# Kernel optimization log

Measured on AMD Instinct MI355X. Metric: run time of the kernel, lower is better.

Reference implementation:

```python
import jax, jax.numpy as jnp
import numpy as np

N_NODES = 50000
N_EDGES = 800000
N_GRAPHS = 512


def gcn_conv(x, W, b, src, dst, n_nodes):
    # Standard PyG GCNConv: linear transform, add self-loops, D^-1/2 (A+I) D^-1/2 aggregation.
    x = x @ W  # [N, out]
    loop = jnp.arange(n_nodes, dtype=src.dtype)
    s = jnp.concatenate([src, loop])  # [E+N]
    d = jnp.concatenate([dst, loop])
    deg = jax.ops.segment_sum(jnp.ones_like(d, dtype=x.dtype), d, num_segments=n_nodes)
    dinv = jnp.where(deg > 0, jax.lax.rsqrt(jnp.maximum(deg, 1e-12)), 0.0)
    norm = dinv[s] * dinv[d]  # [E+N]
    msg = x[s] * norm[:, None]  # gather + scale
    out = jax.ops.segment_sum(msg, d, num_segments=n_nodes)  # scatter-add
    return out + b


def setup_inputs() -> dict:
    key = jax.random.key(0)
    ks = jax.random.split(key, 10)
    x = jax.random.normal(ks[0], (N_NODES, 128), dtype=jnp.float32)
    edge_index = jax.random.randint(ks[1], (2, N_EDGES), 0, N_NODES, dtype=jnp.int64)
    batch = jnp.sort(jax.random.randint(ks[2], (N_NODES,), 0, N_GRAPHS, dtype=jnp.int64))
    y = jax.random.randint(ks[3], (N_GRAPHS,), 0, 4, dtype=jnp.int64)
    W1 = jax.random.normal(ks[4], (128, 64), dtype=jnp.float32) * (1.0 / np.sqrt(128))
    b1 = jnp.zeros((64,), dtype=jnp.float32)
    W2 = jax.random.normal(ks[5], (64, 64), dtype=jnp.float32) * (1.0 / np.sqrt(64))
    b2 = jnp.zeros((64,), dtype=jnp.float32)
    Wfc = jax.random.normal(ks[6], (64, 4), dtype=jnp.float32) * (1.0 / np.sqrt(64))
    bfc = jnp.zeros((4,), dtype=jnp.float32)
    return {"x": x, "edge_index": edge_index, "batch": batch, "y": y,
            "W1": W1, "b1": b1, "W2": W2, "b2": b2, "Wfc": Wfc, "bfc": bfc}


def reference(x, edge_index, batch, y, W1, b1, W2, b2, Wfc, bfc):
    src, dst = edge_index[0], edge_index[1]
    h = jax.nn.relu(gcn_conv(x, W1, b1, src, dst, N_NODES))
    h = jax.nn.relu(gcn_conv(h, W2, b2, src, dst, N_NODES))
    # global mean pool over graph ids
    sums = jax.ops.segment_sum(h, batch, num_segments=N_GRAPHS)  # [G, out]
    cnts = jax.ops.segment_sum(jnp.ones((h.shape[0],), h.dtype), batch, num_segments=N_GRAPHS)
    pooled = sums / jnp.maximum(cnts, 1.0)[:, None]
    logits = pooled @ Wfc + bfc
    logp = jax.nn.log_softmax(logits, axis=1)
    return (logp, y)
```

## Files before the change

### kernel.cpp

```cpp
#include <hip/hip_runtime.h>
#include <hip/hip_fp16.h>
#include <math.h>

#define N_NODES 50000
#define N_EDGES 800000
#define N_GRAPHS 512
#define NBKT 196
#define SENT N_NODES
#define CAP_T 6144
#define CAP_S 8192

typedef float v2f __attribute__((ext_vector_type(2)));

#define OFF_BCNT    0u
#define OFF_DINV    1024u
#define OFF_OFFS2   201216u
#define OFF_TMP     601344u
#define OFF_SORTED  5418240u
#define OFF_XS8_1   11840768u
#define OFF_XS8_2   15041024u
#define OFF_H2      18241280u

__global__ __launch_bounds__(256) void binA(const int* __restrict__ src, const int* __restrict__ dst,
                                            int* __restrict__ bcnt, unsigned int* __restrict__ tmp,
                                            unsigned int* __restrict__ x1, unsigned int* __restrict__ x2) {
    __shared__ int cnt[256];
    __shared__ int lo[256];
    __shared__ int cnt2[256];
    __shared__ int baseg[256];
    __shared__ unsigned int ldsPK[4096];
    __shared__ int ldsDST[4096];
    int t = threadIdx.x;
    cnt[t] = 0; cnt2[t] = 0;
    if (blockIdx.x == 0) {
        if (t < 16) x1[N_NODES * 16 + t] = 0;
        else if (t < 32) x2[N_NODES * 16 + (t - 16)] = 0;
    }
    __syncthreads();
    int e0 = blockIdx.x * 4096;
    int nE = N_EDGES - e0; if (nE > 4096) nE = 4096;
    int sA[16], dA[16];
#pragma unroll
    for (int i = 0; i < 16; ++i) {
        int e = e0 + i * 256 + t;
        if (e < N_EDGES) {
            sA[i] = src[e];
            dA[i] = dst[e];
            atomicAdd(&cnt[dA[i] >> 8], 1);
        } else dA[i] = -1;
    }
    __syncthreads();
    {
        int v = cnt[t];
        lo[t] = v;
        __syncthreads();
        for (int d = 1; d < 256; d <<= 1) {
            int a = (t >= d) ? lo[t - d] : 0;
            __syncthreads();
            lo[t] += a;
            __syncthreads();
        }
        int ex = lo[t] - v;
        __syncthreads();
        lo[t] = ex;
        baseg[t] = (t < NBKT && v) ? atomicAdd(&bcnt[t], v) : 0;
    }
    __syncthreads();
#pragma unroll
    for (int i = 0; i < 16; ++i) {
        if (dA[i] >= 0) {
            int b = dA[i] >> 8;
            int pl = lo[b] + atomicAdd(&cnt2[b], 1);
            ldsPK[pl] = (unsigned int)sA[i] | ((unsigned int)(dA[i] & 255) << 17);
            ldsDST[pl] = b * CAP_T + baseg[b] + (pl - lo[b]);
        }
    }
    __syncthreads();
    for (int p = t; p < nE; p += 256)
        tmp[ldsDST[p]] = ldsPK[p];
}

__global__ __launch_bounds__(256) void binB2(const unsigned int* __restrict__ tmp,
                                             const int* __restrict__ bcnt,
                                             int* __restrict__ sorted, int2* __restrict__ offs2,
                                             float* __restrict__ dinv) {
    __shared__ int cnt[256];
    __shared__ int scn[256];
    __shared__ int cur[256];
    __shared__ int ldsS[CAP_S];
    int b = blockIdx.x, t = threadIdx.x;
    cnt[t] = 0;
    __syncthreads();
    int m = bcnt[b];
    const unsigned int* tp = tmp + b * CAP_T;
    for (int e = t; e < m; e += 256) atomicAdd(&cnt[tp[e] >> 17], 1);
    __syncthreads();
    int deg = cnt[t];
    int pdeg = (deg + 7) & ~7;
    scn[t] = pdeg;
    __syncthreads();
    for (int d = 1; d < 256; d <<= 1) {
        int a = (t >= d) ? scn[t - d] : 0;
        __syncthreads();
        scn[t] += a;
        __syncthreads();
    }
    int begl = scn[t] - pdeg;
    int ptot = scn[255];
    int node = b * 256 + t;
    if (node < N_NODES) {
        offs2[node] = make_int2(b * CAP_S + begl, b * CAP_S + begl + pdeg);
        dinv[node] = rsqrtf(1.0f + (float)deg);
    }
    cur[t] = begl;
    __syncthreads();
    for (int e = t; e < m; e += 256) {
        unsigned int pk = tp[e];
        int p = atomicAdd(&cur[pk >> 17], 1);
        ldsS[p] = (int)(pk & 0x1FFFFu);
    }
    __syncthreads();
    for (int p = cur[t]; p < begl + pdeg; ++p) ldsS[p] = SENT;
    __syncthreads();
    int4* dst4 = (int4*)(sorted + b * CAP_S);
    const int4* src4 = (const int4*)ldsS;
    for (int p = t; p < (ptot >> 2); p += 256) dst4[p] = src4[p];
}

__global__ __launch_bounds__(256) void gemm1(const float* __restrict__ X, const float* __restrict__ W,
                                             const float* __restrict__ dinv, unsigned int* __restrict__ xs8) {
    __shared__ float sW[128 * 64];
    __shared__ float sX[16 * 132];
    int tid = threadIdx.x;
    {
        const float4* ws = (const float4*)W;
        float4* wd = (float4*)sW;
        for (int i = tid; i < 2048; i += 256) wd[i] = ws[i];
    }
    int row0 = blockIdx.x * 16;
    {
        const float4* xs = (const float4*)(X + row0 * 128);
        for (int i = tid; i < 512; i += 256) {
            int r = i >> 5, q = i & 31;
            *(float4*)&sX[r * 132 + 4 * q] = xs[r * 32 + q];
        }
    }
    __syncthreads();
    int r = tid >> 4;
    int cg = (tid & 15) * 4;
    int row = row0 + r;
    float a0 = 0, a1 = 0, a2 = 0, a3 = 0;
#pragma unroll 8
    for (int k = 0; k < 128; ++k) {
        float xv = sX[r * 132 + k];
        float4 w = *(const float4*)&sW[k * 64 + cg];
        a0 += xv * w.x; a1 += xv * w.y; a2 += xv * w.z; a3 += xv * w.w;
    }
    float s = dinv[row];
    unsigned int pk = 0;
    pk = __builtin_amdgcn_cvt_pk_fp8_f32(a0 * s, a1 * s, pk, false);
    pk = __builtin_amdgcn_cvt_pk_fp8_f32(a2 * s, a3 * s, pk, true);
    xs8[row * 16 + (cg >> 2)] = pk;
}

#define ADD_ROW(rv) { \
    v2f f0 = __builtin_amdgcn_cvt_pk_f32_fp8((rv).x, false); \
    v2f f1 = __builtin_amdgcn_cvt_pk_f32_fp8((rv).x, true); \
    v2f f2 = __builtin_amdgcn_cvt_pk_f32_fp8((rv).y, false); \
    v2f f3 = __builtin_amdgcn_cvt_pk_f32_fp8((rv).y, true); \
    a0 += f0.x; a1 += f0.y; a2 += f1.x; a3 += f1.y; \
    a4 += f2.x; a5 += f2.y; a6 += f3.x; a7 += f3.y; }

#define RED_SUB() { \
    a0 += __shfl_xor(a0, 8);  a1 += __shfl_xor(a1, 8);  a2 += __shfl_xor(a2, 8);  a3 += __shfl_xor(a3, 8); \
    a4 += __shfl_xor(a4, 8);  a5 += __shfl_xor(a5, 8);  a6 += __shfl_xor(a6, 8);  a7 += __shfl_xor(a7, 8); \
    a0 += __shfl_xor(a0, 16); a1 += __shfl_xor(a1, 16); a2 += __shfl_xor(a2, 16); a3 += __shfl_xor(a3, 16); \
    a4 += __shfl_xor(a4, 16); a5 += __shfl_xor(a5, 16); a6 += __shfl_xor(a6, 16); a7 += __shfl_xor(a7, 16); \
    a0 += __shfl_xor(a0, 32); a1 += __shfl_xor(a1, 32); a2 += __shfl_xor(a2, 32); a3 += __shfl_xor(a3, 32); \
    a4 += __shfl_xor(a4, 32); a5 += __shfl_xor(a5, 32); a6 += __shfl_xor(a6, 32); a7 += __shfl_xor(a7, 32); }

#define GATHER_BODY(FLUSH_ADV) \
    int lane = threadIdx.x & 63; \
    int sub = lane >> 3, frag = lane & 7; \
    int n0 = wv * 4; \
    int2 oe = offs2[n0 + (lane < 4 ? lane : 3)]; \
    int e0 = __shfl(oe.x, 0), e1 = __shfl(oe.x, 1), e2 = __shfl(oe.x, 2); \
    int e3 = __shfl(oe.x, 3), e4 = __shfl(oe.y, 3); \
    int G   = (e4 - e0) >> 3; \
    int nb1 = (e1 - e0) >> 3, nb2 = (e2 - e0) >> 3, nb3 = (e3 - e0) >> 3; \
    const int* sb = sorted + e0 + sub; \
    int i0 = (0 < G) ? sb[0]  : SENT; \
    int i1 = (1 < G) ? sb[8]  : SENT; \
    int i2 = (2 < G) ? sb[16] : SENT; \
    int i3 = (3 < G) ? sb[24] : SENT; \
    float4 bA = *(const float4*)(bias + frag * 8); \
    float4 bB = *(const float4*)(bias + frag * 8 + 4); \
    int cur = 0; \
    uint2 sv = *(const uint2*)(xs8 + n0 * 64 + frag * 8); \
    float dv = dinv[n0]; \
    float a0 = 0, a1 = 0, a2 = 0, a3 = 0, a4 = 0, a5 = 0, a6 = 0, a7 = 0; \
    for (int g = 0; g < G; g += 4) { \
        uint2 r0 = *(const uint2*)(xs8 + i0 * 64 + frag * 8); \
        uint2 r1 = *(const uint2*)(xs8 + i1 * 64 + frag * 8); \
        uint2 r2 = *(const uint2*)(xs8 + i2 * 64 + frag * 8); \
        uint2 r3 = *(const uint2*)(xs8 + i3 * 64 + frag * 8); \
        const int* np = sb + (g + 4) * 8; \
        i0 = (g + 4 < G) ? np[0]  : SENT; \
        i1 = (g + 5 < G) ? np[8]  : SENT; \
        i2 = (g + 6 < G) ? np[16] : SENT; \
        i3 = (g + 7 < G) ? np[24] : SENT; \
        {   int gg = g; \
            int nxt = BND_NXT(); \
            while (cur < 4 && gg >= nxt) { FLUSH_ADV(); nxt = BND_NXT(); } \
            ADD_ROW(r0); } \
        if (g + 1 < G) { \
            int gg = g + 1; \
            int nxt = BND_NXT(); \
            while (cur < 4 && gg >= nxt) { FLUSH_ADV(); nxt = BND_NXT(); } \
            ADD_ROW(r1); \
        } \
        if (g + 2 < G) { \
            int gg = g + 2; \
            int nxt = BND_NXT(); \
            while (cur < 4 && gg >= nxt) { FLUSH_ADV(); nxt = BND_NXT(); } \
            ADD_ROW(r2); \
        } \
        if (g + 3 < G) { \
            int gg = g + 3; \
            int nxt = BND_NXT(); \
            while (cur < 4 && gg >= nxt) { FLUSH_ADV(); nxt = BND_NXT(); } \
            ADD_ROW(r3); \
        } \
    } \
    while (cur < 4) { FLUSH_ADV(); }

#define BND_NXT() (cur == 0 ? nb1 : cur == 1 ? nb2 : cur == 2 ? nb3 : G)

__global__ __launch_bounds__(256) void gather_fuse(const unsigned char* __restrict__ xs8,
                                                   const int2* __restrict__ offs2,
                                                   const int* __restrict__ sorted,
                                                   const float* __restrict__ dinv,
                                                   const float* __restrict__ bias,
                                                   const float* __restrict__ W2,
                                                   unsigned int* __restrict__ xs8o) {
    __shared__ float sW2[64 * 64];
    __shared__ float sH[16][64];
    {
        const float4* ws = (const float4*)W2;
        float4* wd = (float4*)sW2;
        for (int i = threadIdx.x; i < 1024; i += 256) wd[i] = ws[i];
    }
    int wvl = threadIdx.x >> 6;
    int wv = blockIdx.x * 4 + wvl;

#define FLUSH_LDS() { \
    if (sub == 0) ADD_ROW(sv); \
    RED_SUB(); \
    if (sub == 0) { \
        float4 w0, w1; \
        w0.x = fmaxf(a0 * dv + bA.x, 0.0f); w0.y = fmaxf(a1 * dv + bA.y, 0.0f); \
        w0.z = fmaxf(a2 * dv + bA.z, 0.0f); w0.w = fmaxf(a3 * dv + bA.w, 0.0f); \
        w1.x = fmaxf(a4 * dv + bB.x, 0.0f); w1.y = fmaxf(a5 * dv + bB.y, 0.0f); \
        w1.z = fmaxf(a6 * dv + bB.z, 0.0f); w1.w = fmaxf(a7 * dv + bB.w, 0.0f); \
        *(float4*)&sH[wvl * 4 + cur][frag * 8]     = w0; \
        *(float4*)&sH[wvl * 4 + cur][frag * 8 + 4] = w1; \
    } \
    a0 = a1 = a2 = a3 = a4 = a5 = a6 = a7 = 0.0f; \
    cur++; \
    if (cur < 4) { \
        sv = *(const uint2*)(xs8 + (n0 + cur) * 64 + frag * 8); \
        dv = dinv[n0 + cur]; \
    } }

    GATHER_BODY(FLUSH_LDS)
#undef FLUSH_LDS
    __syncthreads();
    int r = threadIdx.x >> 4;
    int cg = (threadIdx.x & 15) * 4;
    int node = blockIdx.x * 16 + r;
    float b0 = 0, b1 = 0, b2 = 0, b3 = 0;
#pragma unroll 8
    for (int k = 0; k < 64; ++k) {
        float hv = sH[r][k];
        float4 w = *(const float4*)&sW2[k * 64 + cg];
        b0 += hv * w.x; b1 += hv * w.y; b2 += hv * w.z; b3 += hv * w.w;
    }
    float s = dinv[node];
    unsigned int pk = 0;
    pk = __builtin_amdgcn_cvt_pk_fp8_f32(b0 * s, b1 * s, pk, false);
    pk = __builtin_amdgcn_cvt_pk_fp8_f32(b2 * s, b3 * s, pk, true);
    xs8o[node * 16 + (cg >> 2)] = pk;
}

__global__ __launch_bounds__(256) void gather_h2(const unsigned char* __restrict__ xs8,
                                                 const int2* __restrict__ offs2,
                                                 const int* __restrict__ sorted,
                                                 const float* __restrict__ dinv,
                                                 const float* __restrict__ bias,
                                                 __half* __restrict__ h2) {
    int wv = blockIdx.x * 4 + (threadIdx.x >> 6);

#define FLUSH_H2() { \
    if (sub == 0) ADD_ROW(sv); \
    RED_SUB(); \
    if (sub == 0) { \
        float v0 = fmaxf(a0 * dv + bA.x, 0.0f), v1 = fmaxf(a1 * dv + bA.y, 0.0f); \
        float v2 = fmaxf(a2 * dv + bA.z, 0.0f), v3 = fmaxf(a3 * dv + bA.w, 0.0f); \
        float v4 = fmaxf(a4 * dv + bB.x, 0.0f), v5 = fmaxf(a5 * dv + bB.y, 0.0f); \
        float v6 = fmaxf(a6 * dv + bB.z, 0.0f), v7 = fmaxf(a7 * dv + bB.w, 0.0f); \
        __half2 p0 = __floats2half2_rn(v0, v1), p1 = __floats2half2_rn(v2, v3); \
        __half2 p2 = __floats2half2_rn(v4, v5), p3 = __floats2half2_rn(v6, v7); \
        uint4 pk; \
        pk.x = *(unsigned int*)&p0; pk.y = *(unsigned int*)&p1; \
        pk.z = *(unsigned int*)&p2; pk.w = *(unsigned int*)&p3; \
        *(uint4*)(h2 + (n0 + cur) * 64 + frag * 8) = pk; \
    } \
    a0 = a1 = a2 = a3 = a4 = a5 = a6 = a7 = 0.0f; \
    cur++; \
    if (cur < 4) { \
        sv = *(const uint2*)(xs8 + (n0 + cur) * 64 + frag * 8); \
        dv = dinv[n0 + cur]; \
    } }

    GATHER_BODY(FLUSH_H2)
#undef FLUSH_H2
}

__device__ __forceinline__ int lower_bound(const int* __restrict__ a, int n, int v) {
    int lo = 0, hi = n;
    while (lo < hi) { int m = (lo + hi) >> 1; if (a[m] < v) lo = m + 1; else hi = m; }
    return lo;
}

__global__ __launch_bounds__(256) void pool_head(const __half* __restrict__ h2,
                                                 const int* __restrict__ batch,
                                                 const float* __restrict__ Wfc, const float* __restrict__ bfc,
                                                 const int* __restrict__ y, float* __restrict__ out) {
    __shared__ int s_beg, s_end;
    __shared__ float sh[4][64];
    __shared__ float pl[64];
    __shared__ float lg[4];
    int g = blockIdx.x;
    int t = threadIdx.x;
    if (t == 0) s_beg = lower_bound(batch, N_NODES, g);
    if (t == 1) s_end = lower_bound(batch, N_NODES, g + 1);
    __syncthreads();
    int beg = s_beg, end = s_end;
    int f = t & 63, seg = t >> 6;
    float s = 0.0f;
    for (int r = beg + seg; r < end; r += 4) s += __half2float(h2[r * 64 + f]);
    sh[seg][f] = s;
    __syncthreads();
    if (t < 64) {
        float p = sh[0][t] + sh[1][t] + sh[2][t] + sh[3][t];
        pl[t] = p / fmaxf((float)(end - beg), 1.0f);
    }
    __syncthreads();
    if (t < 4) {
        float l = bfc[t];
#pragma unroll
        for (int k = 0; k < 64; ++k) l += pl[k] * Wfc[k * 4 + t];
        lg[t] = l;
    }
    __syncthreads();
    if (t == 0) {
        float l0 = lg[0], l1 = lg[1], l2 = lg[2], l3 = lg[3];
        float m = fmaxf(fmaxf(l0, l1), fmaxf(l2, l3));
        float ss = expf(l0 - m) + expf(l1 - m) + expf(l2 - m) + expf(l3 - m);
        float lse = m + logf(ss);
        out[g * 4 + 0] = l0 - lse;
        out[g * 4 + 1] = l1 - lse;
        out[g * 4 + 2] = l2 - lse;
        out[g * 4 + 3] = l3 - lse;
        out[N_GRAPHS * 4 + g] = (float)y[g];
    }
}

extern "C" void kernel_launch(void* const* d_in, const int* in_sizes, int n_in,
                              void* d_out, int out_size, void* d_ws, size_t ws_size,
                              hipStream_t stream) {
    const float* x     = (const float*)d_in[0];
    const int*   ei    = (const int*)d_in[1];
    const int*   batch = (const int*)d_in[2];
    const int*   y     = (const int*)d_in[3];
    const float* W1    = (const float*)d_in[4];
    const float* b1    = (const float*)d_in[5];
    const float* W2    = (const float*)d_in[6];
    const float* b2    = (const float*)d_in[7];
    const float* Wfc   = (const float*)d_in[8];
    const float* bfc   = (const float*)d_in[9];
    float* out = (float*)d_out;

    const int* src = ei;
    const int* dst = ei + N_EDGES;

    char* wsb = (char*)d_ws;
    int*          bcnt   = (int*)(wsb + OFF_BCNT);
    float*        dinv   = (float*)(wsb + OFF_DINV);
    int2*         offs2  = (int2*)(wsb + OFF_OFFS2);
    unsigned int* tmp    = (unsigned int*)(wsb + OFF_TMP);
    int*          sorted = (int*)(wsb + OFF_SORTED);
    unsigned int* xs8_1  = (unsigned int*)(wsb + OFF_XS8_1);
    unsigned int* xs8_2  = (unsigned int*)(wsb + OFF_XS8_2);
    __half*       h2     = (__half*)(wsb + OFF_H2);

    hipMemsetAsync(bcnt, 0, 1024u, stream);

    binA<<<NBKT, 256, 0, stream>>>(src, dst, bcnt, tmp, xs8_1, xs8_2);
    binB2<<<NBKT, 256, 0, stream>>>(tmp, bcnt, sorted, offs2, dinv);

    gemm1<<<N_NODES / 16, 256, 0, stream>>>(x, W1, dinv, xs8_1);
    gather_fuse<<<N_NODES / 16, 256, 0, stream>>>((const unsigned char*)xs8_1, offs2, sorted,
                                                  dinv, b1, W2, xs8_2);
    gather_h2<<<N_NODES / 16, 256, 0, stream>>>((const unsigned char*)xs8_2, offs2, sorted,
                                                dinv, b2, h2);

    pool_head<<<N_GRAPHS, 256, 0, stream>>>(h2, batch, Wfc, bfc, y, out);
}
```

Before: 196.7 us.

## Merge bucket sort and first GEMM into one launch via global degree histogram

Adds a global per-node degree histogram built with atomics in binA, so the first GEMM can compute dinv itself instead of waiting for the bucket sort kernel. The bucket-sort blocks and GEMM blocks now run in one combined launch, which removes a kernel boundary and lets the two independent stages overlap. The cost is 800K extra global atomics in binA, a larger memset, and shared memory sized for the bigger of the two roles.

```diff
diff --git a/kernel.cpp b/kernel.cpp
--- a/kernel.cpp
+++ b/kernel.cpp
@@ -13,16 +13,18 @@
 typedef float v2f __attribute__((ext_vector_type(2)));
 
 #define OFF_BCNT    0u
-#define OFF_DINV    1024u
-#define OFF_OFFS2   201216u
-#define OFF_TMP     601344u
-#define OFF_SORTED  5418240u
-#define OFF_XS8_1   11840768u
-#define OFF_XS8_2   15041024u
-#define OFF_H2      18241280u
+#define OFF_HIST    1024u
+#define OFF_DINV    201216u
+#define OFF_OFFS2   401408u
+#define OFF_TMP     801536u
+#define OFF_SORTED  5618432u
+#define OFF_XS8_1   12040960u
+#define OFF_XS8_2   15241216u
+#define OFF_H2      18441472u
 
 __global__ __launch_bounds__(256) void binA(const int* __restrict__ src, const int* __restrict__ dst,
                                             int* __restrict__ bcnt, unsigned int* __restrict__ tmp,
+                                            int* __restrict__ hist,
                                             unsigned int* __restrict__ x1, unsigned int* __restrict__ x2) {
     __shared__ int cnt[256];
     __shared__ int lo[256];
@@ -47,6 +49,7 @@
             sA[i] = src[e];
             dA[i] = dst[e];
             atomicAdd(&cnt[dA[i] >> 8], 1);
+            atomicAdd(&hist[dA[i]], 1);
         } else dA[i] = -1;
     }
     __syncthreads();
@@ -80,74 +83,73 @@
         tmp[ldsDST[p]] = ldsPK[p];
 }
 
-__global__ __launch_bounds__(256) void binB2(const unsigned int* __restrict__ tmp,
+__global__ __launch_bounds__(256) void prep2(const unsigned int* __restrict__ tmp,
                                              const int* __restrict__ bcnt,
                                              int* __restrict__ sorted, int2* __restrict__ offs2,
-                                             float* __restrict__ dinv) {
-    __shared__ int cnt[256];
-    __shared__ int scn[256];
-    __shared__ int cur[256];
-    __shared__ int ldsS[CAP_S];
-    int b = blockIdx.x, t = threadIdx.x;
-    cnt[t] = 0;
-    __syncthreads();
-    int m = bcnt[b];
-    const unsigned int* tp = tmp + b * CAP_T;
-    for (int e = t; e < m; e += 256) atomicAdd(&cnt[tp[e] >> 17], 1);
-    __syncthreads();
-    int deg = cnt[t];
-    int pdeg = (deg + 7) & ~7;
-    scn[t] = pdeg;
-    __syncthreads();
-    for (int d = 1; d < 256; d <<= 1) {
-        int a = (t >= d) ? scn[t - d] : 0;
-        __syncthreads();
-        scn[t] += a;
-        __syncthreads();
-    }
-    int begl = scn[t] - pdeg;
-    int ptot = scn[255];
-    int node = b * 256 + t;
-    if (node < N_NODES) {
-        offs2[node] = make_int2(b * CAP_S + begl, b * CAP_S + begl + pdeg);
-        dinv[node] = rsqrtf(1.0f + (float)deg);
-    }
-    cur[t] = begl;
-    __syncthreads();
-    for (int e = t; e < m; e += 256) {
-        unsigned int pk = tp[e];
-        int p = atomicAdd(&cur[pk >> 17], 1);
-        ldsS[p] = (int)(pk & 0x1FFFFu);
-    }
-    __syncthreads();
-    for (int p = cur[t]; p < begl + pdeg; ++p) ldsS[p] = SENT;
-    __syncthreads();
-    int4* dst4 = (int4*)(sorted + b * CAP_S);
-    const int4* src4 = (const int4*)ldsS;
-    for (int p = t; p < (ptot >> 2); p += 256) dst4[p] = src4[p];
-}
-
-__global__ __launch_bounds__(256) void gemm1(const float* __restrict__ X, const float* __restrict__ W,
-                                             const float* __restrict__ dinv, unsigned int* __restrict__ xs8) {
-    __shared__ float sW[128 * 64];
-    __shared__ float sX[16 * 132];
-    int tid = threadIdx.x;
+                                             const float* __restrict__ X, const float* __restrict__ W,
+                                             const int* __restrict__ hist, float* __restrict__ dinv,
+                                             unsigned int* __restrict__ xs8) {
+    __shared__ float smem[10304];
+    int bid = blockIdx.x, t = threadIdx.x;
+    if (bid < NBKT) {
+        int* cnt = (int*)smem;
+        int* scn = cnt + 256;
+        int* cur = scn + 256;
+        int* ldsS = cur + 256;
+        cnt[t] = 0;
+        __syncthreads();
+        int m = bcnt[bid];
+        const unsigned int* tp = tmp + bid * CAP_T;
+        for (int e = t; e < m; e += 256) atomicAdd(&cnt[tp[e] >> 17], 1);
+        __syncthreads();
+        int deg = cnt[t];
+        int pdeg = (deg + 7) & ~7;
+        scn[t] = pdeg;
+        __syncthreads();
+        for (int d = 1; d < 256; d <<= 1) {
+            int a = (t >= d) ? scn[t - d] : 0;
+            __syncthreads();
+            scn[t] += a;
+            __syncthreads();
+        }
+        int begl = scn[t] - pdeg;
+        int ptot = scn[255];
+        int node = bid * 256 + t;
+        if (node < N_NODES)
+            offs2[node] = make_int2(bid * CAP_S + begl, bid * CAP_S + begl + pdeg);
+        cur[t] = begl;
+        __syncthreads();
+        for (int e = t; e < m; e += 256) {
+            unsigned int pk = tp[e];
+            int p = atomicAdd(&cur[pk >> 17], 1);
+            ldsS[p] = (int)(pk & 0x1FFFFu);
+        }
+        __syncthreads();
+        for (int p = cur[t]; p < begl + pdeg; ++p) ldsS[p] = SENT;
+        __syncthreads();
+        int4* dst4 = (int4*)(sorted + bid * CAP_S);
+        const int4* src4 = (const int4*)ldsS;
+        for (int p = t; p < (ptot >> 2); p += 256) dst4[p] = src4[p];
+        return;
+    }
+    float* sW = smem;
+    float* sX = smem + 8192;
     {
         const float4* ws = (const float4*)W;
         float4* wd = (float4*)sW;
-        for (int i = tid; i < 2048; i += 256) wd[i] = ws[i];
-    }
-    int row0 = blockIdx.x * 16;
+        for (int i = t; i < 2048; i += 256) wd[i] = ws[i];
+    }
+    int row0 = (bid - NBKT) * 16;
     {
         const float4* xs = (const float4*)(X + row0 * 128);
-        for (int i = tid; i < 512; i += 256) {
+        for (int i = t; i < 512; i += 256) {
             int r = i >> 5, q = i & 31;
             *(float4*)&sX[r * 132 + 4 * q] = xs[r * 32 + q];
         }
     }
     __syncthreads();
-    int r = tid >> 4;
-    int cg = (tid & 15) * 4;
+    int r = t >> 4;
+    int cg = (t & 15) * 4;
     int row = row0 + r;
     float a0 = 0, a1 = 0, a2 = 0, a3 = 0;
 #pragma unroll 8
@@ -156,7 +158,8 @@
         float4 w = *(const float4*)&sW[k * 64 + cg];
         a0 += xv * w.x; a1 += xv * w.y; a2 += xv * w.z; a3 += xv * w.w;
     }
-    float s = dinv[row];
+    float s = rsqrtf(1.0f + (float)hist[row]);
+    if ((t & 15) == 0) dinv[row] = s;
     unsigned int pk = 0;
     pk = __builtin_amdgcn_cvt_pk_fp8_f32(a0 * s, a1 * s, pk, false);
     pk = __builtin_amdgcn_cvt_pk_fp8_f32(a2 * s, a3 * s, pk, true);
@@ -396,6 +399,7 @@
 
     char* wsb = (char*)d_ws;
     int*          bcnt   = (int*)(wsb + OFF_BCNT);
+    int*          hist   = (int*)(wsb + OFF_HIST);
     float*        dinv   = (float*)(wsb + OFF_DINV);
     int2*         offs2  = (int2*)(wsb + OFF_OFFS2);
     unsigned int* tmp    = (unsigned int*)(wsb + OFF_TMP);
@@ -404,12 +408,11 @@
     unsigned int* xs8_2  = (unsigned int*)(wsb + OFF_XS8_2);
     __half*       h2     = (__half*)(wsb + OFF_H2);
 
-    hipMemsetAsync(bcnt, 0, 1024u, stream);
-
-    binA<<<NBKT, 256, 0, stream>>>(src, dst, bcnt, tmp, xs8_1, xs8_2);
-    binB2<<<NBKT, 256, 0, stream>>>(tmp, bcnt, sorted, offs2, dinv);
-
-    gemm1<<<N_NODES / 16, 256, 0, stream>>>(x, W1, dinv, xs8_1);
+    hipMemsetAsync(wsb, 0, 201216u, stream);
+
+    binA<<<NBKT, 256, 0, stream>>>(src, dst, bcnt, tmp, hist, xs8_1, xs8_2);
+    prep2<<<NBKT + N_NODES / 16, 256, 0, stream>>>(tmp, bcnt, sorted, offs2,
+                                                   x, W1, hist, dinv, xs8_1);
     gather_fuse<<<N_NODES / 16, 256, 0, stream>>>((const unsigned char*)xs8_1, offs2, sorted,
                                                   dinv, b1, W2, xs8_2);
     gather_h2<<<N_NODES / 16, 256, 0, stream>>>((const unsigned char*)xs8_2, offs2, sorted,
```

Measured after the change: 217.4 us. +10.5%, slower.
